# Kernel tuning notes

Hardware: AMD Instinct MI355X
Metric: run time of the kernel (lower is better)

The kernel has to match this reference:

```python
import jax, jax.numpy as jnp
import numpy as np

LEAK = 0.2          # LeakyReLU negative slope
NEG = -9e15         # mask fill value from the original module
N, FIN, FOUT = 8192, 256, 128


def setup_inputs() -> dict:
    key = jax.random.key(0)
    k1, k2, k3, k4 = jax.random.split(key, 4)
    x = jax.random.normal(k1, (N, FIN), dtype=jnp.float32)
    # dense 0/1 adjacency mask, p(edge) ~= 0.5
    adj = jax.random.randint(k2, (N, N), 0, 2, dtype=jnp.int32)
    # xavier_uniform with gain sqrt(2)
    gW = np.sqrt(2.0) * np.sqrt(6.0 / (FIN + FOUT))
    W = jax.random.uniform(k3, (FIN, FOUT), dtype=jnp.float32, minval=-gW, maxval=gW)
    ga = np.sqrt(2.0) * np.sqrt(6.0 / (FOUT + 1))
    a = jax.random.uniform(k4, (FOUT, 1), dtype=jnp.float32, minval=-ga, maxval=ga)
    return {"x": x, "adj": adj, "W": W, "a": a}


def reference(x, adj, W, a):
    # h = X W                                     [N, FOUT]
    h = x @ W
    # alpha_j = a . h_j  -- the original's h.repeat(N,1) @ a reduces to this,
    # since every row block of the repeat is identical.
    alpha = jnp.squeeze(h @ a, axis=-1)           # [N]
    e = jax.nn.leaky_relu(alpha, LEAK)            # [N]
    # e_ij depends only on column j; broadcast across rows, then mask.
    scores = jnp.where(adj > 0, e[None, :], NEG)  # [N, N]
    attention = jax.nn.softmax(scores, axis=1)    # [N, N]
    # dropout: eval mode (training=False) -> identity
    h_prime = attention @ h                       # [N, FOUT]
    return h_prime
```

## Files before the change

### kernel.cpp

```cpp
#include <hip/hip_runtime.h>
#include <hip/hip_bf16.h>

#define NN 8192
#define FIN 256
#define FOUT 128

typedef __attribute__((ext_vector_type(8))) short short8;
typedef __attribute__((ext_vector_type(4))) float f32x4;
typedef unsigned short u16;

__device__ inline u16 bf16r(float v) {
  return __builtin_bit_cast(u16, __float2bfloat16(v));
}

__global__ __launch_bounds__(256) void k_h_e(const float* __restrict__ x,
                                             const float* __restrict__ W,
                                             const float* __restrict__ a,
                                             float* __restrict__ h,
                                             float* __restrict__ e) {
  __shared__ float xs[32 * 256];
  __shared__ float ap[4][16];
  const int t = threadIdx.x;
  const int r0 = blockIdx.x * 32;

  const float4* xg = (const float4*)(x + (size_t)r0 * FIN);
  float4* xs4 = (float4*)xs;
#pragma unroll
  for (int p = 0; p < 8; ++p) xs4[p * 256 + t] = xg[p * 256 + t];
  __syncthreads();

  const int f = t & 127;
  const int half = t >> 7;
  float acc[16];
#pragma unroll
  for (int i = 0; i < 16; ++i) acc[i] = 0.f;

  const float4* xsr = (const float4*)(xs + half * 16 * 256);
  for (int k4 = 0; k4 < 64; ++k4) {
    float w0 = W[(k4 * 4 + 0) * FOUT + f];
    float w1 = W[(k4 * 4 + 1) * FOUT + f];
    float w2 = W[(k4 * 4 + 2) * FOUT + f];
    float w3 = W[(k4 * 4 + 3) * FOUT + f];
#pragma unroll
    for (int i = 0; i < 16; ++i) {
      float4 xv = xsr[i * 64 + k4];
      acc[i] = fmaf(xv.x, w0, acc[i]);
      acc[i] = fmaf(xv.y, w1, acc[i]);
      acc[i] = fmaf(xv.z, w2, acc[i]);
      acc[i] = fmaf(xv.w, w3, acc[i]);
    }
  }
#pragma unroll
  for (int i = 0; i < 16; ++i)
    h[(size_t)(r0 + half * 16 + i) * FOUT + f] = acc[i];

  const float af = a[f];
  float part[16];
#pragma unroll
  for (int i = 0; i < 16; ++i) part[i] = acc[i] * af;
#pragma unroll
  for (int i = 0; i < 16; ++i) {
#pragma unroll
    for (int off = 32; off >= 1; off >>= 1) part[i] += __shfl_xor(part[i], off);
  }
  const int wvid = t >> 6;
  if ((t & 63) == 0) {
#pragma unroll
    for (int i = 0; i < 16; ++i) ap[wvid][i] = part[i];
  }
  __syncthreads();
  if (t < 32) {
    int i = t & 15, hh = t >> 4;
    float alpha = ap[hh * 2][i] + ap[hh * 2 + 1][i];
    e[r0 + hh * 16 + i] = alpha > 0.f ? alpha : 0.2f * alpha;
  }
}

__global__ __launch_bounds__(1024) void k_max(const float* __restrict__ e,
                                              float* __restrict__ M) {
  __shared__ float red[16];
  const int t = threadIdx.x;
  float m = -3.4e38f;
  for (int i = t; i < NN; i += 1024) m = fmaxf(m, e[i]);
#pragma unroll
  for (int off = 32; off >= 1; off >>= 1) m = fmaxf(m, __shfl_xor(m, off));
  if ((t & 63) == 0) red[t >> 6] = m;
  __syncthreads();
  if (t == 0) {
    float mm = red[0];
#pragma unroll
    for (int i = 1; i < 16; ++i) mm = fmaxf(mm, red[i]);
    *M = mm;
  }
}

__global__ __launch_bounds__(256) void k_gw(const float* __restrict__ h,
                                            const float* __restrict__ e,
                                            const float* __restrict__ Mp,
                                            float* __restrict__ w,
                                            u16* __restrict__ gT) {
  __shared__ float wsh[64];
  __shared__ u16 gsh[64][132];
  const int t = threadIdx.x;
  const int j0 = blockIdx.x * 64;
  const float M = *Mp;
  if (t < 64) {
    float wv = __expf(e[j0 + t] - M);
    wsh[t] = wv;
    w[j0 + t] = wv;
  }
  __syncthreads();
#pragma unroll
  for (int p = 0; p < 8; ++p) {
    int lin = p * 256 + t;
    int j = lin >> 5;
    int fc = (lin & 31) * 4;
    float4 hv = *(const float4*)(h + (size_t)(j0 + j) * FOUT + fc);
    float wv = wsh[j];
    ushort4 g4;
    g4.x = bf16r(hv.x * wv);
    g4.y = bf16r(hv.y * wv);
    g4.z = bf16r(hv.z * wv);
    g4.w = bf16r(hv.w * wv);
    *(ushort4*)&gsh[j][fc] = g4;
  }
  __syncthreads();
  const int f = t >> 1;
  const int jc = (t & 1) * 32;
  u16* dst = gT + (size_t)f * NN + j0 + jc;
#pragma unroll
  for (int q = 0; q < 8; ++q) {
    ushort4 v;
    v.x = gsh[jc + q * 4 + 0][f];
    v.y = gsh[jc + q * 4 + 1][f];
    v.z = gsh[jc + q * 4 + 2][f];
    v.w = gsh[jc + q * 4 + 3][f];
    *(ushort4*)(dst + q * 4) = v;
  }
}

__global__ __launch_bounds__(512) void k_gemm(const int* __restrict__ adj,
                                              const u16* __restrict__ gT,
                                              const float* __restrict__ w,
                                              float* __restrict__ out) {
  __shared__ u16 Ash[2][32 * 64];
  __shared__ u16 Bsh[2][128 * 64];
  __shared__ float denom_sh[32];

  const int t = threadIdx.x;
  const int lane = t & 63;
  const int wvid = t >> 6;
  const int wr = wvid >> 2;
  const int wc = wvid & 3;
  const int r0 = blockIdx.x * 32;

  const int ar = t >> 4;
  const int ako = (t & 15) * 4;
  const int* adjrow = adj + (size_t)(r0 + ar) * NN + ako;
  const int bfr = t >> 3;
  const int bck = (t & 7) * 8;

  f32x4 acc0 = {0.f, 0.f, 0.f, 0.f};
  f32x4 acc1 = {0.f, 0.f, 0.f, 0.f};
  float dpart = 0.f;

  int4 av;
  float4 wq;
  short8 bb0, bb1;

  auto LOAD = [&](int kt) {
    av = *(const int4*)(adjrow + kt * 64);
    wq = *(const float4*)(w + kt * 64 + ako);
    const u16* gp = gT + (size_t)bfr * NN + kt * 64 + bck;
    bb0 = *(const short8*)gp;
    bb1 = *(const short8*)(gp + (size_t)64 * NN);
  };
  auto STORE = [&](int buf) {
    dpart += (av.x ? wq.x : 0.f) + (av.y ? wq.y : 0.f) +
             (av.z ? wq.z : 0.f) + (av.w ? wq.w : 0.f);
    ushort4 a4;
    a4.x = av.x ? (u16)0x3F80 : (u16)0;
    a4.y = av.y ? (u16)0x3F80 : (u16)0;
    a4.z = av.z ? (u16)0x3F80 : (u16)0;
    a4.w = av.w ? (u16)0x3F80 : (u16)0;
    int abyte = ar * 128 + ((ako * 2) ^ ((ar & 7) << 4));
    *(ushort4*)((char*)&Ash[buf][0] + abyte) = a4;
    int bbyte = bfr * 128 + ((bck * 2) ^ ((bfr & 7) << 4));
    *(short8*)((char*)&Bsh[buf][0] + bbyte) = bb0;
    *(short8*)((char*)&Bsh[buf][0] + bbyte + 64 * 128) = bb1;
  };
  auto COMPUTE = [&](int buf) {
    const int swz = (lane & 7) << 4;
    const int arow = wr * 16 + (lane & 15);
    const int bcol = wc * 32 + (lane & 15);
#pragma unroll
    for (int kc = 0; kc < 2; ++kc) {
      int kbyte = kc * 64 + (lane >> 4) * 16;
      short8 afr = *(const short8*)((const char*)&Ash[buf][0] + arow * 128 + (kbyte ^ swz));
      short8 b0  = *(const short8*)((const char*)&Bsh[buf][0] + bcol * 128 + (kbyte ^ swz));
      short8 b1  = *(const short8*)((const char*)&Bsh[buf][0] + (bcol + 16) * 128 + (kbyte ^ swz));
      acc0 = __builtin_amdgcn_mfma_f32_16x16x32_bf16(afr, b0, acc0, 0, 0, 0);
      acc1 = __builtin_amdgcn_mfma_f32_16x16x32_bf16(afr, b1, acc1, 0, 0, 0);
    }
  };

  LOAD(0);
  STORE(0);
  LOAD(1);
  __syncthreads();
  for (int kt = 0; kt < NN / 64; ++kt) {
    int buf = kt & 1;
    if (kt + 1 < NN / 64) STORE(buf ^ 1);
    if (kt + 2 < NN / 64) LOAD(kt + 2);
    COMPUTE(buf);
    __syncthreads();
  }

  dpart += __shfl_xor(dpart, 1);
  dpart += __shfl_xor(dpart, 2);
  dpart += __shfl_xor(dpart, 4);
  dpart += __shfl_xor(dpart, 8);
  if ((t & 15) == 0) denom_sh[ar] = dpart;
  __syncthreads();

#pragma unroll
  for (int q = 0; q < 4; ++q) {
    int row = wr * 16 + (lane >> 4) * 4 + q;
    float d = denom_sh[row];
    int col = wc * 32 + (lane & 15);
    out[(size_t)(r0 + row) * FOUT + col] = acc0[q] / d;
    out[(size_t)(r0 + row) * FOUT + col + 16] = acc1[q] / d;
  }
}

extern "C" void kernel_launch(void* const* d_in, const int* in_sizes, int n_in,
                              void* d_out, int out_size, void* d_ws, size_t ws_size,
                              hipStream_t stream) {
  const float* x = (const float*)d_in[0];
  const int* adj = (const int*)d_in[1];
  const float* W = (const float*)d_in[2];
  const float* a = (const float*)d_in[3];
  float* out = (float*)d_out;

  char* ws = (char*)d_ws;
  float* h = (float*)ws;
  float* e = (float*)(ws + (size_t)4 * 1024 * 1024);
  float* wexp = (float*)(ws + (size_t)4 * 1024 * 1024 + 32 * 1024);
  float* M = (float*)(ws + (size_t)4 * 1024 * 1024 + 64 * 1024);
  u16* gT = (u16*)(ws + (size_t)4 * 1024 * 1024 + 128 * 1024);

  hipLaunchKernelGGL(k_h_e, dim3(NN / 32), dim3(256), 0, stream, x, W, a, h, e);
  hipLaunchKernelGGL(k_max, dim3(1), dim3(1024), 0, stream, e, M);
  hipLaunchKernelGGL(k_gw, dim3(NN / 64), dim3(256), 0, stream, h, e, M, wexp, gT);
  hipLaunchKernelGGL(k_gemm, dim3(NN / 32), dim3(512), 0, stream, adj, gT, wexp, out);
}
```

Measured before the change: 114.1 us.

## Fuse prep kernels, drop global max, and split-K the attention GEMM

Folds h computation, exp weighting and the transposed bf16 write into one prep kernel. The global max reduction is replaced by exp of the score clamped at 80, which keeps the result unchanged because the softmax is shift-invariant. The main GEMM is split into two K halves across blockIdx.y to double the block count, and a new combine kernel sums the partial numerators and denominators. This removes two launches and the h round-trip through memory, at the cost of writing and re-reading the partials and of a numeric risk if scores are large or if every exp underflows.

```diff
diff --git a/kernel.cpp b/kernel.cpp
--- a/kernel.cpp
+++ b/kernel.cpp
@@ -4,6 +4,8 @@
 #define NN 8192
 #define FIN 256
 #define FOUT 128
+#define KSPLIT 2
+#define KHALF (NN / KSPLIT)
 
 typedef __attribute__((ext_vector_type(8))) short short8;
 typedef __attribute__((ext_vector_type(4))) float f32x4;
@@ -13,13 +15,15 @@
   return __builtin_bit_cast(u16, __float2bfloat16(v));
 }
 
-__global__ __launch_bounds__(256) void k_h_e(const float* __restrict__ x,
-                                             const float* __restrict__ W,
-                                             const float* __restrict__ a,
-                                             float* __restrict__ h,
-                                             float* __restrict__ e) {
+__global__ __launch_bounds__(256) void k_prep(const float* __restrict__ x,
+                                              const float* __restrict__ W,
+                                              const float* __restrict__ a,
+                                              float* __restrict__ wexp,
+                                              u16* __restrict__ gT) {
   __shared__ float xs[32 * 256];
   __shared__ float ap[4][16];
+  __shared__ float wsh[32];
+  __shared__ u16 gsh[32][132];
   const int t = threadIdx.x;
   const int r0 = blockIdx.x * 32;
 
@@ -50,9 +54,6 @@
       acc[i] = fmaf(xv.w, w3, acc[i]);
     }
   }
-#pragma unroll
-  for (int i = 0; i < 16; ++i)
-    h[(size_t)(r0 + half * 16 + i) * FOUT + f] = acc[i];
 
   const float af = a[f];
   float part[16];
@@ -72,77 +73,39 @@
   if (t < 32) {
     int i = t & 15, hh = t >> 4;
     float alpha = ap[hh * 2][i] + ap[hh * 2 + 1][i];
-    e[r0 + hh * 16 + i] = alpha > 0.f ? alpha : 0.2f * alpha;
-  }
-}
-
-__global__ __launch_bounds__(1024) void k_max(const float* __restrict__ e,
-                                              float* __restrict__ M) {
-  __shared__ float red[16];
-  const int t = threadIdx.x;
-  float m = -3.4e38f;
-  for (int i = t; i < NN; i += 1024) m = fmaxf(m, e[i]);
-#pragma unroll
-  for (int off = 32; off >= 1; off >>= 1) m = fmaxf(m, __shfl_xor(m, off));
-  if ((t & 63) == 0) red[t >> 6] = m;
-  __syncthreads();
-  if (t == 0) {
-    float mm = red[0];
-#pragma unroll
-    for (int i = 1; i < 16; ++i) mm = fmaxf(mm, red[i]);
-    *M = mm;
-  }
-}
-
-__global__ __launch_bounds__(256) void k_gw(const float* __restrict__ h,
-                                            const float* __restrict__ e,
-                                            const float* __restrict__ Mp,
-                                            float* __restrict__ w,
-                                            u16* __restrict__ gT) {
-  __shared__ float wsh[64];
-  __shared__ u16 gsh[64][132];
-  const int t = threadIdx.x;
-  const int j0 = blockIdx.x * 64;
-  const float M = *Mp;
-  if (t < 64) {
-    float wv = __expf(e[j0 + t] - M);
+    float ee = alpha > 0.f ? alpha : 0.2f * alpha;
+    float wv = __expf(fminf(ee, 80.f));
     wsh[t] = wv;
-    w[j0 + t] = wv;
-  }
-  __syncthreads();
-#pragma unroll
-  for (int p = 0; p < 8; ++p) {
-    int lin = p * 256 + t;
-    int j = lin >> 5;
-    int fc = (lin & 31) * 4;
-    float4 hv = *(const float4*)(h + (size_t)(j0 + j) * FOUT + fc);
-    float wv = wsh[j];
-    ushort4 g4;
-    g4.x = bf16r(hv.x * wv);
-    g4.y = bf16r(hv.y * wv);
-    g4.z = bf16r(hv.z * wv);
-    g4.w = bf16r(hv.w * wv);
-    *(ushort4*)&gsh[j][fc] = g4;
-  }
-  __syncthreads();
-  const int f = t >> 1;
-  const int jc = (t & 1) * 32;
-  u16* dst = gT + (size_t)f * NN + j0 + jc;
-#pragma unroll
-  for (int q = 0; q < 8; ++q) {
+    wexp[r0 + t] = wv;
+  }
+  __syncthreads();
+
+#pragma unroll
+  for (int i = 0; i < 16; ++i) {
+    int row = half * 16 + i;
+    gsh[row][f] = bf16r(acc[i] * wsh[row]);
+  }
+  __syncthreads();
+
+  const int ff = t >> 1;
+  const int jc = (t & 1) * 16;
+  u16* dst = gT + (size_t)ff * NN + r0 + jc;
+#pragma unroll
+  for (int q = 0; q < 4; ++q) {
     ushort4 v;
-    v.x = gsh[jc + q * 4 + 0][f];
-    v.y = gsh[jc + q * 4 + 1][f];
-    v.z = gsh[jc + q * 4 + 2][f];
-    v.w = gsh[jc + q * 4 + 3][f];
+    v.x = gsh[jc + q * 4 + 0][ff];
+    v.y = gsh[jc + q * 4 + 1][ff];
+    v.z = gsh[jc + q * 4 + 2][ff];
+    v.w = gsh[jc + q * 4 + 3][ff];
     *(ushort4*)(dst + q * 4) = v;
   }
 }
 
-__global__ __launch_bounds__(512) void k_gemm(const int* __restrict__ adj,
-                                              const u16* __restrict__ gT,
-                                              const float* __restrict__ w,
-                                              float* __restrict__ out) {
+__global__ __launch_bounds__(512, 4) void k_gemm(const int* __restrict__ adj,
+                                                 const u16* __restrict__ gT,
+                                                 const float* __restrict__ w,
+                                                 float* __restrict__ numer,
+                                                 float* __restrict__ denom) {
   __shared__ u16 Ash[2][32 * 64];
   __shared__ u16 Bsh[2][128 * 64];
   __shared__ float denom_sh[32];
@@ -153,12 +116,16 @@
   const int wr = wvid >> 2;
   const int wc = wvid & 3;
   const int r0 = blockIdx.x * 32;
+  const int ks = blockIdx.y;
+  const size_t kbase = (size_t)ks * KHALF;
 
   const int ar = t >> 4;
   const int ako = (t & 15) * 4;
-  const int* adjrow = adj + (size_t)(r0 + ar) * NN + ako;
+  const int* adjrow = adj + (size_t)(r0 + ar) * NN + kbase + ako;
+  const float* wp = w + kbase + ako;
   const int bfr = t >> 3;
   const int bck = (t & 7) * 8;
+  const u16* gTb = gT + kbase + bck;
 
   f32x4 acc0 = {0.f, 0.f, 0.f, 0.f};
   f32x4 acc1 = {0.f, 0.f, 0.f, 0.f};
@@ -170,8 +137,8 @@
 
   auto LOAD = [&](int kt) {
     av = *(const int4*)(adjrow + kt * 64);
-    wq = *(const float4*)(w + kt * 64 + ako);
-    const u16* gp = gT + (size_t)bfr * NN + kt * 64 + bck;
+    wq = *(const float4*)(wp + kt * 64);
+    const u16* gp = gTb + (size_t)bfr * NN + kt * 64;
     bb0 = *(const short8*)gp;
     bb1 = *(const short8*)(gp + (size_t)64 * NN);
   };
@@ -204,14 +171,15 @@
     }
   };
 
+  const int NT = KHALF / 64;
   LOAD(0);
   STORE(0);
   LOAD(1);
   __syncthreads();
-  for (int kt = 0; kt < NN / 64; ++kt) {
+  for (int kt = 0; kt < NT; ++kt) {
     int buf = kt & 1;
-    if (kt + 1 < NN / 64) STORE(buf ^ 1);
-    if (kt + 2 < NN / 64) LOAD(kt + 2);
+    if (kt + 1 < NT) STORE(buf ^ 1);
+    if (kt + 2 < NT) LOAD(kt + 2);
     COMPUTE(buf);
     __syncthreads();
   }
@@ -226,11 +194,30 @@
 #pragma unroll
   for (int q = 0; q < 4; ++q) {
     int row = wr * 16 + (lane >> 4) * 4 + q;
-    float d = denom_sh[row];
     int col = wc * 32 + (lane & 15);
-    out[(size_t)(r0 + row) * FOUT + col] = acc0[q] / d;
-    out[(size_t)(r0 + row) * FOUT + col + 16] = acc1[q] / d;
-  }
+    float* np = numer + ((size_t)ks * NN + r0 + row) * FOUT + col;
+    np[0] = acc0[q];
+    np[16] = acc1[q];
+  }
+  if (t < 32) denom[(size_t)ks * NN + r0 + t] = denom_sh[t];
+}
+
+__global__ __launch_bounds__(256) void k_comb(const float* __restrict__ numer,
+                                              const float* __restrict__ denom,
+                                              float* __restrict__ out) {
+  const int idx = blockIdx.x * 256 + threadIdx.x;
+  const int row = idx >> 5;
+  const int fc = (idx & 31) * 4;
+  float4 n0 = *(const float4*)(numer + (size_t)row * FOUT + fc);
+  float4 n1 = *(const float4*)(numer + (size_t)(NN + row) * FOUT + fc);
+  float d = denom[row] + denom[NN + row];
+  float inv = 1.0f / d;
+  float4 o;
+  o.x = (n0.x + n1.x) * inv;
+  o.y = (n0.y + n1.y) * inv;
+  o.z = (n0.z + n1.z) * inv;
+  o.w = (n0.w + n1.w) * inv;
+  *(float4*)(out + (size_t)row * FOUT + fc) = o;
 }
 
 extern "C" void kernel_launch(void* const* d_in, const int* in_sizes, int n_in,
@@ -243,14 +230,14 @@
   float* out = (float*)d_out;
 
   char* ws = (char*)d_ws;
-  float* h = (float*)ws;
-  float* e = (float*)(ws + (size_t)4 * 1024 * 1024);
-  float* wexp = (float*)(ws + (size_t)4 * 1024 * 1024 + 32 * 1024);
-  float* M = (float*)(ws + (size_t)4 * 1024 * 1024 + 64 * 1024);
-  u16* gT = (u16*)(ws + (size_t)4 * 1024 * 1024 + 128 * 1024);
-
-  hipLaunchKernelGGL(k_h_e, dim3(NN / 32), dim3(256), 0, stream, x, W, a, h, e);
-  hipLaunchKernelGGL(k_max, dim3(1), dim3(1024), 0, stream, e, M);
-  hipLaunchKernelGGL(k_gw, dim3(NN / 64), dim3(256), 0, stream, h, e, M, wexp, gT);
-  hipLaunchKernelGGL(k_gemm, dim3(NN / 32), dim3(512), 0, stream, adj, gT, wexp, out);
-}
+  float* wexp = (float*)ws;
+  u16* gT = (u16*)(ws + 64 * 1024);
+  float* numer = (float*)(ws + 4 * 1024 * 1024);
+  float* denom = (float*)(ws + 12 * 1024 * 1024);
+
+  hipLaunchKernelGGL(k_prep, dim3(NN / 32), dim3(256), 0, stream, x, W, a, wexp, gT);
+  hipLaunchKernelGGL(k_gemm, dim3(NN / 32, KSPLIT), dim3(512), 0, stream, adj, gT, wexp,
+                     numer, denom);
+  hipLaunchKernelGGL(k_comb, dim3((NN * FOUT / 4) / 256), dim3(256), 0, stream, numer,
+                     denom, out);
+}
```

Result: faster. 96.44 us (-15.4%).
